# Kernel tuning notes

Measured on AMD Instinct MI355X. Metric: run time of the kernel, lower is better.

The kernel has to match this reference:

```python
import jax, jax.numpy as jnp
import numpy as np

N_NODES = 100000
N_EDGES = 1000000
HEADS = 3
NEG_SLOPE_ATTN = 0.2   # DGL EdgeGATConv default negative_slope
NEG_SLOPE_MLP = 0.01   # torch nn.LeakyReLU default


def _edge_softmax(e, dst, num_nodes):
    # softmax over incoming edges of each destination node; e: [E,H]
    m = jax.ops.segment_max(e, dst, num_segments=num_nodes)
    ex = jnp.exp(e - m[dst])
    s = jax.ops.segment_sum(ex, dst, num_segments=num_nodes)
    return ex / s[dst]


def _edge_gat(h, ef, src, dst, Wfc, Wedge, al, ar, ae, Wres, b, D):
    # Faithful to dgl.nn.EdgeGATConv (residual=True, bias=True defaults).
    N = h.shape[0]
    H = HEADS
    ft = (h @ Wfc).reshape(N, H, D)        # [N,H,D] projected node feats
    fe = (ef @ Wedge).reshape(-1, H, D)    # [E,H,D] projected edge feats
    el = jnp.einsum('nhd,hd->nh', ft, al)
    er = jnp.einsum('nhd,hd->nh', ft, ar)
    ee = jnp.einsum('ehd,hd->eh', fe, ae)
    e = jax.nn.leaky_relu(el[src] + er[dst] + ee, NEG_SLOPE_ATTN)  # [E,H]
    a = _edge_softmax(e, dst, N)                                   # [E,H]
    rst = jax.ops.segment_sum(ft[src] * a[..., None], dst, num_segments=N)
    # residual projection + bias (DGL defaults residual=True, bias=True)
    return rst + (h @ Wres).reshape(N, H, D) + b.reshape(1, H, D)


def _forward(node_feats, edge_feats,
             W1, We1, al1, ar1, ae1, Wr1, b1,
             W2, We2, al2, ar2, ae2, Wr2, b2,
             W3, We3, al3, ar3, ae3, Wr3, b3,
             L1a_w, L1a_b, L1b_w, L1b_b, L1c_w, L1c_b, L2_w, L2_b,
             src, dst):
    h1 = _edge_gat(node_feats, edge_feats, src, dst, W1, We1, al1, ar1, ae1, Wr1, b1, 8)
    h2 = _edge_gat(h1.mean(axis=1), edge_feats, src, dst, W2, We2, al2, ar2, ae2, Wr2, b2, 16)
    h3 = _edge_gat(h2.mean(axis=1), edge_feats, src, dst, W3, We3, al3, ar3, ae3, Wr3, b3, 32)
    # linear1 MLP head applied per (node, head)
    x = jax.nn.leaky_relu(h3 @ L1a_w + L1a_b, NEG_SLOPE_MLP)   # [N,H,16]
    x = jax.nn.leaky_relu(x @ L1b_w + L1b_b, NEG_SLOPE_MLP)    # [N,H,4]
    x = x @ L1c_w + L1c_b                                       # [N,H,1]
    x = x.reshape(x.shape[0], -1) @ L2_w + L2_b                 # [N,1]
    return jnp.max(x, axis=0)                                   # [1]


def setup_inputs() -> dict:
    key = jax.random.key(0)
    ks = iter(jax.random.split(key, 64))

    def nrm(shape, scale=0.1):
        return jax.random.normal(next(ks), shape, dtype=jnp.float32) * scale

    inp = {
        'node_feats': jax.random.normal(next(ks), (N_NODES, 6), dtype=jnp.float32),
        'edge_feats': jax.random.uniform(next(ks), (N_EDGES, 1), dtype=jnp.float32),
    }
    dims = [(6, 8), (8, 16), (16, 32)]
    for i, (din, dout) in enumerate(dims, start=1):
        inp[f'W{i}'] = nrm((din, HEADS * dout))
        inp[f'We{i}'] = nrm((1, HEADS * dout))
        inp[f'al{i}'] = nrm((HEADS, dout))
        inp[f'ar{i}'] = nrm((HEADS, dout))
        inp[f'ae{i}'] = nrm((HEADS, dout))
        inp[f'Wr{i}'] = nrm((din, HEADS * dout))
        inp[f'b{i}'] = nrm((HEADS * dout,))
    inp['L1a_w'] = nrm((32, 16)); inp['L1a_b'] = nrm((16,))
    inp['L1b_w'] = nrm((16, 4));  inp['L1b_b'] = nrm((4,))
    inp['L1c_w'] = nrm((4, 1));   inp['L1c_b'] = nrm((1,))
    inp['L2_w'] = nrm((HEADS, 1)); inp['L2_b'] = nrm((1,))
    inp['src'] = jax.random.randint(next(ks), (N_EDGES,), 0, N_NODES, dtype=jnp.int32)
    inp['dst'] = jax.random.randint(next(ks), (N_EDGES,), 0, N_NODES, dtype=jnp.int32)
    return inp


def reference(node_feats, edge_feats,
              W1, We1, al1, ar1, ae1, Wr1, b1,
              W2, We2, al2, ar2, ae2, Wr2, b2,
              W3, We3, al3, ar3, ae3, Wr3, b3,
              L1a_w, L1a_b, L1b_w, L1b_b, L1c_w, L1c_b, L2_w, L2_b,
              src, dst):
    return _forward(node_feats, edge_feats,
                    W1, We1, al1, ar1, ae1, Wr1, b1,
                    W2, We2, al2, ar2, ae2, Wr2, b2,
                    W3, We3, al3, ar3, ae3, Wr3, b3,
                    L1a_w, L1a_b, L1b_w, L1b_b, L1c_w, L1c_b, L2_w, L2_b,
                    src, dst)
```

## Files before the change

kernel.cpp:

```cpp
#include <hip/hip_runtime.h>
#include <hip/hip_fp16.h>
#include <math.h>

#define NN 100000
#define NE 1000000
#define NCHUNK 160
#define CHUNK (NE/NCHUNK)
#define NODE_RANGE (NN/8)
#define CAPS 32

typedef unsigned int   u32;
typedef unsigned short u16;

__device__ __forceinline__ float lrelu(float x, float sl){ return x >= 0.f ? x : sl*x; }

__device__ __forceinline__ void atomicMaxF(float* a, float v){
    if (v >= 0.f) atomicMax((int*)a, __float_as_int(v));
    else          atomicMin((unsigned int*)a, __float_as_uint(v));
}

__global__ void __launch_bounds__(256) kInit(int* __restrict__ deg, float* __restrict__ out){
    int i = blockIdx.x*256 + threadIdx.x;
    if (i < NN + 1) deg[i] = 0;
    if (i == 0) out[0] = -INFINITY;
}

__global__ void __launch_bounds__(256) kScatterX1(const int* __restrict__ src,
        const int* __restrict__ dst, const float* __restrict__ ef,
        int* __restrict__ deg, u32* __restrict__ pack,
        int* __restrict__ ovfc, int4* __restrict__ ovf){
    const int xcd  = blockIdx.x & 7;
    const int base = (blockIdx.x >> 3)*CHUNK;
    for (int e = base + threadIdx.x; e < base + CHUNK; e += 256){
        int d = __builtin_nontemporal_load(dst + e);
        if (d / NODE_RANGE == xcd){
            int s   = __builtin_nontemporal_load(src + e);
            float fv = __builtin_nontemporal_load(ef + e);
            int pos = atomicAdd(&deg[d], 1);
            if (pos < CAPS){
                u32 rec = ((u32)s << 15) | (u32)(fv*32767.f + 0.5f);
                pack[(size_t)d*CAPS + pos] = rec;
            } else {
                int o = atomicAdd(ovfc, 1);
                ovf[o] = make_int4(d, s, __float_as_int(fv), 0);
            }
        }
    }
}

template<int DIN, int DINP, int D, bool WRM>
__device__ void coefBody(const float* __restrict__ Wfc, const float* __restrict__ al,
                         const float* __restrict__ ar, const float* __restrict__ We,
                         const float* __restrict__ ae, const float* __restrict__ Wres,
                         const float* __restrict__ bias,
                         float* __restrict__ q, float* __restrict__ r, float* __restrict__ ce,
                         float* __restrict__ wrm, float* __restrict__ bm){
    int t = threadIdx.x;
    for (int i = t; i < 3*DINP; i += 256){
        int hd = i/DINP, k = i - hd*DINP;
        float qa = 0.f, ra = 0.f;
        if (k < DIN){
            for (int d = 0; d < D; ++d){
                float w = Wfc[k*3*D + hd*D + d];
                qa += w*al[hd*D+d];
                ra += w*ar[hd*D+d];
            }
        }
        q[i] = qa; r[i] = ra;
    }
    if (t < 3){
        float c = 0.f;
        for (int d = 0; d < D; ++d) c += We[t*D+d]*ae[t*D+d];
        ce[t] = c;
    }
    if (WRM){
        for (int i = t; i < DIN*D; i += 256){
            int k = i/D, d = i - k*D;
            wrm[i] = (Wres[k*3*D+d] + Wres[k*3*D+D+d] + Wres[k*3*D+2*D+d])*(1.f/3.f);
        }
        for (int i = t; i < D; i += 256)
            bm[i] = (bias[i] + bias[D+i] + bias[2*D+i])*(1.f/3.f);
    }
}

__global__ void __launch_bounds__(256) kPrep(
    const float* W1, const float* al1, const float* ar1, const float* We1,
    const float* ae1, const float* Wr1, const float* b1,
    const float* W2, const float* al2, const float* ar2, const float* We2,
    const float* ae2, const float* Wr2, const float* b2,
    const float* W3, const float* al3, const float* ar3, const float* We3,
    const float* ae3, const float* Wr3, const float* b3,
    const float* L1a_w, const float* L1a_b,
    float* coef, float* FA, float* FR, float* C0,
    const float* __restrict__ nf, u32* __restrict__ ntab1, float* __restrict__ er3a)
{
    if (blockIdx.x == 0){
        coefBody<6,8,8,true>(W1, al1, ar1, We1, ae1, Wr1, b1,
            coef+0, coef+24, coef+48, coef+52, coef+100);
    } else if (blockIdx.x == 1){
        coefBody<8,8,16,true>(W2, al2, ar2, We2, ae2, Wr2, b2,
            coef+108, coef+132, coef+156, coef+160, coef+288);
    } else if (blockIdx.x == 2){
        coefBody<16,16,32,false>(W3, al3, ar3, We3, ae3, Wr3, b3,
            coef+304, coef+352, coef+400, nullptr, nullptr);
    } else if (blockIdx.x == 3){
        int t = threadIdx.x;
        for (int i = t; i < 768; i += 256){
            int hd = i >> 8, rem = i & 255;
            int k = rem >> 4, ii = rem & 15;
            float a = 0.f, r = 0.f;
            for (int d = 0; d < 32; ++d){
                float w = L1a_w[d*16 + ii];
                a += W3[k*96 + hd*32 + d]*w;
                r += Wr3[k*96 + hd*32 + d]*w;
            }
            FA[i] = a; FR[i] = r;
        }
        if (t < 48){
            int hd = t >> 4, ii = t & 15;
            float c = L1a_b[ii];
            for (int d = 0; d < 32; ++d) c += b3[hd*32 + d]*L1a_w[d*16 + ii];
            C0[t] = c;
        }
    } else {
        __shared__ float r1s[24];
        int t = threadIdx.x;
        if (t < 24){
            int hd = t >> 3, k = t & 7;
            float ra = 0.f;
            if (k < 6)
                for (int d = 0; d < 8; ++d) ra += W1[k*24 + hd*8 + d]*ar1[hd*8 + d];
            r1s[t] = ra;
        }
        __syncthreads();
        int n = (blockIdx.x - 4)*256 + t;
        if (n >= NN) return;
        float h[6];
        #pragma unroll
        for (int k = 0; k < 6; ++k) h[k] = nf[(size_t)n*6 + k];
        __half2 p0 = __floats2half2_rn(h[0], h[1]);
        __half2 p1 = __floats2half2_rn(h[2], h[3]);
        __half2 p2 = __floats2half2_rn(h[4], h[5]);
        __half2 p3 = __floats2half2_rn(0.f, 0.f);
        uint4 row;
        row.x = *(u32*)&p0; row.y = *(u32*)&p1; row.z = *(u32*)&p2; row.w = *(u32*)&p3;
        *(uint4*)(ntab1 + (size_t)n*4) = row;
        #pragma unroll
        for (int hd = 0; hd < 3; ++hd){
            float er = 0.f;
            #pragma unroll
            for (int k = 0; k < 6; ++k) er += r1s[hd*8+k]*h[k];
            er3a[(size_t)n*3+hd] = er;
        }
    }
}

template<int DINP, int DINR, int D, bool AGG>
__global__ void __launch_bounds__(256) kNode(
    const int* __restrict__ deg, const u32* __restrict__ pack,
    const int* __restrict__ ovfc, const int4* __restrict__ ovf,
    const u32* __restrict__ ntab,
    const float* __restrict__ er3, const float* __restrict__ qc,
    const float* __restrict__ cep, const float* __restrict__ hres,
    const float* __restrict__ Wfc, const float* __restrict__ Wr2,
    const float* __restrict__ b2,
    float* __restrict__ hmean_o, u32* __restrict__ ntab_next,
    float* __restrict__ er3_next, const float* __restrict__ rnext,
    float* __restrict__ agg_o)
{
    constexpr int KS   = DINP/4;
    constexpr int ROWU = DINP/2;
    constexpr int D4   = D/4;
    const int tid  = threadIdx.x;
    const int lid  = tid & 63;
    const int lane = tid & 3;
    const int n    = (blockIdx.x*256 + tid) >> 2;
    const bool alive = n < NN;

    int dg = 0;
    float e0 = 0.f, e1 = 0.f, e2 = 0.f;
    if (alive){
        dg = deg[n]; if (dg > CAPS) dg = CAPS;
        e0 = er3[(size_t)n*3+0]; e1 = er3[(size_t)n*3+1]; e2 = er3[(size_t)n*3+2];
    }
    const float c0 = cep[0], c1 = cep[1], c2 = cep[2];
    float q[3*KS];
    #pragma unroll
    for (int hd = 0; hd < 3; ++hd)
        #pragma unroll
        for (int ks = 0; ks < KS; ++ks)
            q[hd*KS+ks] = qc[hd*DINP + lane*KS + ks];

    float acc[3*KS];
    #pragma unroll
    for (int v = 0; v < 3*KS; ++v) acc[v] = 0.f;
    float s0 = 0.f, s1 = 0.f, s2 = 0.f;

    auto rowLoad = [&](int sv, u32& w0, u32& w1){
        const u32* rp = ntab + (size_t)sv*ROWU + lane*(KS/2);
        if constexpr (KS == 2){ w0 = rp[0]; w1 = 0u; }
        else { uint2 t2 = *(const uint2*)rp; w0 = t2.x; w1 = t2.y; }
    };
    auto edgeCompute = [&](float fv, u32 w0, u32 w1){
        float hv[KS];
        float2 f = __half22float2(*(__half2*)&w0);
        hv[0] = f.x; hv[1] = f.y;
        if constexpr (KS == 4){
            f = __half22float2(*(__half2*)&w1);
            hv[2] = f.x; hv[3] = f.y;
        }
        float l0 = 0.f, l1 = 0.f, l2 = 0.f;
        #pragma unroll
        for (int ks = 0; ks < KS; ++ks){
            l0 += q[ks]*hv[ks]; l1 += q[KS+ks]*hv[ks]; l2 += q[2*KS+ks]*hv[ks];
        }
        l0 += __shfl_xor(l0,1); l0 += __shfl_xor(l0,2);
        l1 += __shfl_xor(l1,1); l1 += __shfl_xor(l1,2);
        l2 += __shfl_xor(l2,1); l2 += __shfl_xor(l2,2);
        float x0 = __expf(lrelu(l0 + e0 + c0*fv, 0.2f));
        float x1 = __expf(lrelu(l1 + e1 + c1*fv, 0.2f));
        float x2 = __expf(lrelu(l2 + e2 + c2*fv, 0.2f));
        s0 += x0; s1 += x1; s2 += x2;
        #pragma unroll
        for (int ks = 0; ks < KS; ++ks){
            acc[ks]      += x0*hv[ks];
            acc[KS+ks]   += x1*hv[ks];
            acc[2*KS+ks] += x2*hv[ks];
        }
    };

    int p = n*CAPS;
    const int re = p + dg;
    while (p + 1 < re){
        u32 ra = pack[p], rb = pack[p+1];
        u32 a0, a1, b0, b1;
        rowLoad((int)(ra >> 15), a0, a1);
        rowLoad((int)(rb >> 15), b0, b1);
        edgeCompute((float)(ra & 0x7fffu)*(1.f/32767.f), a0, a1);
        edgeCompute((float)(rb & 0x7fffu)*(1.f/32767.f), b0, b1);
        p += 2;
    }
    if (p < re){
        u32 ra = pack[p];
        u32 a0, a1;
        rowLoad((int)(ra >> 15), a0, a1);
        edgeCompute((float)(ra & 0x7fffu)*(1.f/32767.f), a0, a1);
    }

    int nov = ovfc[0];
    for (int i = 0; i < nov; ++i){
        int4 o = ovf[i];
        if (alive && o.x == n){
            u32 a0, a1;
            rowLoad(o.y, a0, a1);
            edgeCompute(__int_as_float(o.z), a0, a1);
        }
    }

    float i0 = s0 > 0.f ? 1.f/s0 : 0.f;
    float i1 = s1 > 0.f ? 1.f/s1 : 0.f;
    float i2 = s2 > 0.f ? 1.f/s2 : 0.f;
    if constexpr (!AGG){ i0 *= (1.f/3.f); i1 *= (1.f/3.f); i2 *= (1.f/3.f); }
    #pragma unroll
    for (int ks = 0; ks < KS; ++ks){
        acc[ks] *= i0; acc[KS+ks] *= i1; acc[2*KS+ks] *= i2;
    }

    if constexpr (AGG){
        if (alive){
            #pragma unroll
            for (int hd = 0; hd < 3; ++hd){
                float4 v = make_float4(acc[hd*KS+0], acc[hd*KS+1], acc[hd*KS+2], acc[hd*KS+3]);
                *(float4*)(agg_o + (size_t)n*48 + hd*16 + lane*4) = v;
            }
        }
        return;
    } else {
        float hsl[KS];
        #pragma unroll
        for (int ks = 0; ks < KS; ++ks){
            int k = lane*KS + ks;
            hsl[ks] = (alive && k < DINR) ? hres[(size_t)n*DINR + k] : 0.f;
        }
        float hm[D4];
        #pragma unroll
        for (int i = 0; i < D4; ++i) hm[i] = b2[lane*D4 + i];
        #pragma unroll
        for (int r = 0; r < 4; ++r){
            int sl = (lid & ~3) | ((lid + r) & 3);
            int kb = ((lane + r) & 3)*KS;
            float as[3*KS], hs[KS];
            #pragma unroll
            for (int v = 0; v < 3*KS; ++v) as[v] = __shfl(acc[v], sl);
            #pragma unroll
            for (int v = 0; v < KS; ++v) hs[v] = __shfl(hsl[v], sl);
            #pragma unroll
            for (int ks = 0; ks < KS; ++ks){
                int k = kb + ks;
                if (DINP == DINR || k < DINR){
                    #pragma unroll
                    for (int i = 0; i < D4; ++i){
                        int d = lane*D4 + i;
                        hm[i] += as[ks]     *Wfc[k*3*D + d]
                               + as[KS+ks]  *Wfc[k*3*D + D + d]
                               + as[2*KS+ks]*Wfc[k*3*D + 2*D + d]
                               + hs[ks]     *Wr2[k*D + d];
                    }
                }
            }
        }
        if (alive){
            #pragma unroll
            for (int i = 0; i < D4; ++i)
                hmean_o[(size_t)n*D + lane*D4 + i] = hm[i];
            #pragma unroll
            for (int w = 0; w < D4/2; ++w){
                __half2 hh = __floats2half2_rn(hm[2*w], hm[2*w+1]);
                ntab_next[(size_t)n*(D/2) + lane*(D4/2) + w] = *(u32*)&hh;
            }
        }
        float p0 = 0.f, p1 = 0.f, p2 = 0.f;
        #pragma unroll
        for (int i = 0; i < D4; ++i){
            int d = lane*D4 + i;
            p0 += rnext[0*D + d]*hm[i];
            p1 += rnext[1*D + d]*hm[i];
            p2 += rnext[2*D + d]*hm[i];
        }
        p0 += __shfl_xor(p0,1); p0 += __shfl_xor(p0,2);
        p1 += __shfl_xor(p1,1); p1 += __shfl_xor(p1,2);
        p2 += __shfl_xor(p2,1); p2 += __shfl_xor(p2,2);
        if (alive && lane < 3){
            float v = (lane == 0) ? p0 : ((lane == 1) ? p1 : p2);
            er3_next[(size_t)n*3 + lane] = v;
        }
    }
}

__global__ void __launch_bounds__(256) kFin3(
    const float* __restrict__ agg,
    const float* __restrict__ hres,
    const float* __restrict__ FAg, const float* __restrict__ FRg,
    const float* __restrict__ C0g,
    const float* __restrict__ L1b_w, const float* __restrict__ L1b_b,
    const float* __restrict__ L1c_w, const float* __restrict__ L1c_b,
    const float* __restrict__ L2_w, const float* __restrict__ L2_b,
    float* __restrict__ out)
{
    __shared__ float fa[768];
    __shared__ float fr[768];
    __shared__ float lb[64];
    __shared__ float cc[64];
    const int tid = threadIdx.x;
    for (int i = tid; i < 768; i += 256){ fa[i] = FAg[i]; fr[i] = FRg[i]; }
    if (tid < 48) cc[tid] = C0g[tid];
    if (tid < 64) lb[tid] = L1b_w[tid];
    if (tid < 4)  cc[48+tid] = L1b_b[tid];
    if (tid < 4)  cc[52+tid] = L1c_w[tid];
    if (tid == 0) cc[56] = L1c_b[0];
    if (tid < 3)  cc[57+tid] = L2_w[tid];
    if (tid == 0) cc[60] = L2_b[0];
    __syncthreads();

    const int t  = blockIdx.x*256 + tid;
    const int n  = t >> 2;
    const int hd = t & 3;
    const bool alive = n < NN;

    float y = 0.f;
    if (alive && hd < 3){
        float ag[16], hr[16];
        const float4* ag4 = (const float4*)(agg + (size_t)n*48 + hd*16);
        const float4* hr4 = (const float4*)(hres + (size_t)n*16);
        #pragma unroll
        for (int w = 0; w < 4; ++w){
            float4 a = ag4[w], h = hr4[w];
            ag[4*w]=a.x; ag[4*w+1]=a.y; ag[4*w+2]=a.z; ag[4*w+3]=a.w;
            hr[4*w]=h.x; hr[4*w+1]=h.y; hr[4*w+2]=h.z; hr[4*w+3]=h.w;
        }
        float x1[16];
        #pragma unroll
        for (int i = 0; i < 16; ++i) x1[i] = cc[hd*16 + i];
        #pragma unroll
        for (int k = 0; k < 16; ++k){
            const float a = ag[k], h = hr[k];
            const float* fap = fa + hd*256 + k*16;
            const float* frp = fr + hd*256 + k*16;
            #pragma unroll
            for (int i = 0; i < 16; ++i)
                x1[i] += a*fap[i] + h*frp[i];
        }
        #pragma unroll
        for (int i = 0; i < 16; ++i) x1[i] = lrelu(x1[i], 0.01f);
        float x2[4];
        #pragma unroll
        for (int ii = 0; ii < 4; ++ii){
            float a = cc[48+ii];
            #pragma unroll
            for (int i = 0; i < 16; ++i) a += x1[i]*lb[i*4+ii];
            x2[ii] = lrelu(a, 0.01f);
        }
        float v = cc[56];
        #pragma unroll
        for (int ii = 0; ii < 4; ++ii) v += x2[ii]*cc[52+ii];
        y = v*cc[57+hd];
    }
    y += __shfl_xor(y, 1);
    y += __shfl_xor(y, 2);
    float ymax = alive ? (y + cc[60]) : -INFINITY;

    __shared__ float red[256];
    red[tid] = ymax;
    __syncthreads();
    for (int o = 128; o > 0; o >>= 1){
        if (tid < o) red[tid] = fmaxf(red[tid], red[tid+o]);
        __syncthreads();
    }
    if (tid == 0) atomicMaxF(out, red[0]);
}

extern "C" void kernel_launch(void* const* d_in, const int* in_sizes, int n_in,
                              void* d_out, int out_size, void* d_ws, size_t ws_size,
                              hipStream_t stream) {
    const float* nf  = (const float*)d_in[0];
    const float* ef  = (const float*)d_in[1];
    const float* W1  = (const float*)d_in[2];
    const float* We1 = (const float*)d_in[3];
    const float* al1 = (const float*)d_in[4];
    const float* ar1 = (const float*)d_in[5];
    const float* ae1 = (const float*)d_in[6];
    const float* Wr1 = (const float*)d_in[7];
    const float* b1  = (const float*)d_in[8];
    const float* W2  = (const float*)d_in[9];
    const float* We2 = (const float*)d_in[10];
    const float* al2 = (const float*)d_in[11];
    const float* ar2 = (const float*)d_in[12];
    const float* ae2 = (const float*)d_in[13];
    const float* Wr2 = (const float*)d_in[14];
    const float* b2  = (const float*)d_in[15];
    const float* W3  = (const float*)d_in[16];
    const float* We3 = (const float*)d_in[17];
    const float* al3 = (const float*)d_in[18];
    const float* ar3 = (const float*)d_in[19];
    const float* ae3 = (const float*)d_in[20];
    const float* Wr3 = (const float*)d_in[21];
    const float* b3  = (const float*)d_in[22];
    const float* L1a_w = (const float*)d_in[23];
    const float* L1a_b = (const float*)d_in[24];
    const float* L1b_w = (const float*)d_in[25];
    const float* L1b_b = (const float*)d_in[26];
    const float* L1c_w = (const float*)d_in[27];
    const float* L1c_b = (const float*)d_in[28];
    const float* L2_w  = (const float*)d_in[29];
    const float* L2_b  = (const float*)d_in[30];
    const int* src = (const int*)d_in[31];
    const int* dst = (const int*)d_in[32];
    float* out = (float*)d_out;

    float* ws = (float*)d_ws;
    u32* ntab1 = (u32*)ws;
    u32* ntab2 = ntab1 + (size_t)NN*4;
    u32* ntab3 = ntab2 + (size_t)NN*4;
    float* f   = (float*)(ntab3 + (size_t)NN*8);
    float* hm2  = f;  f += (size_t)NN*8;
    float* hm3  = f;  f += (size_t)NN*16;
    float* aggb = f;  f += (size_t)NN*48;
    float* er3a = f;  f += (size_t)NN*3;
    float* er3b = f;  f += (size_t)NN*3;
    float* coef = f;  f += 512;
    float* FAb = f;  f += 768;
    float* FRb = f;  f += 768;
    float* C0b = f;  f += 64;
    int* deg  = (int*)f;
    int* ovfc = deg + NN;
    int4* ovf = (int4*)(ovfc + 4);
    u32* pack = (u32*)(ovf + 4096);

    const int gI = (NN + 1 + 255)/256;
    const int gX = NCHUNK*8;
    const int gP = 4 + (NN + 255)/256;
    const int gT = (NN*4 + 255)/256;

    kInit<<<gI,256,0,stream>>>(deg, out);

    kScatterX1<<<gX,256,0,stream>>>(src, dst, ef, deg, pack, ovfc, ovf);

    kPrep<<<gP,256,0,stream>>>(W1, al1, ar1, We1, ae1, Wr1, b1,
                               W2, al2, ar2, We2, ae2, Wr2, b2,
                               W3, al3, ar3, We3, ae3, Wr3, b3,
                               L1a_w, L1a_b, coef, FAb, FRb, C0b,
                               nf, ntab1, er3a);

    kNode<8,6,8,false><<<gT,256,0,stream>>>(deg, pack, ovfc, ovf, ntab1, er3a,
        coef+0, coef+48, nf, W1, coef+52, coef+100,
        hm2, ntab2, er3b, coef+132, nullptr);

    kNode<8,8,16,false><<<gT,256,0,stream>>>(deg, pack, ovfc, ovf, ntab2, er3b,
        coef+108, coef+156, hm2, W2, coef+160, coef+288,
        hm3, ntab3, er3a, coef+352, nullptr);

    kNode<16,16,32,true><<<gT,256,0,stream>>>(deg, pack, ovfc, ovf, ntab3, er3a,
        coef+304, coef+400, hm3, W3, nullptr, nullptr,
        nullptr, nullptr, nullptr, nullptr, aggb);

    kFin3<<<gT,256,0,stream>>>(aggb, hm3, FAb, FRb, C0b,
        L1b_w, L1b_b, L1c_w, L1c_b, L2_w, L2_b, out);
}
```

Measured before the change: 192.6 us.

## Partition edges into per-XCD buckets before scattering into CSR slots

```diff
diff --git a/kernel.cpp b/kernel.cpp
--- a/kernel.cpp
+++ b/kernel.cpp
@@ -4,13 +4,16 @@
 
 #define NN 100000
 #define NE 1000000
-#define NCHUNK 160
-#define CHUNK (NE/NCHUNK)
+#define NCHUNKP 320
+#define CHUNKP (NE/NCHUNKP)
 #define NODE_RANGE (NN/8)
 #define CAPS 32
-
-typedef unsigned int   u32;
-typedef unsigned short u16;
+#define BKCAP 160000
+#define PB 64
+
+typedef unsigned int        u32;
+typedef unsigned short      u16;
+typedef unsigned long long  u64;
 
 __device__ __forceinline__ float lrelu(float x, float sl){ return x >= 0.f ? x : sl*x; }
 
@@ -19,31 +22,64 @@
     else          atomicMin((unsigned int*)a, __float_as_uint(v));
 }
 
-__global__ void __launch_bounds__(256) kInit(int* __restrict__ deg, float* __restrict__ out){
+__global__ void __launch_bounds__(256) kInit(int* __restrict__ deg, int* __restrict__ bkcur,
+                                             float* __restrict__ out){
     int i = blockIdx.x*256 + threadIdx.x;
     if (i < NN + 1) deg[i] = 0;
+    if (i < 8) bkcur[i] = i*BKCAP;
     if (i == 0) out[0] = -INFINITY;
 }
 
-__global__ void __launch_bounds__(256) kScatterX1(const int* __restrict__ src,
+__global__ void __launch_bounds__(256) kPart(const int* __restrict__ src,
         const int* __restrict__ dst, const float* __restrict__ ef,
-        int* __restrict__ deg, u32* __restrict__ pack,
+        u64* __restrict__ bkt, int* __restrict__ bkcur){
+    __shared__ u64 stg[CHUNKP];
+    __shared__ int cnt[8], lbase[8], gofs[8], cur[8];
+    const int base = blockIdx.x*CHUNKP;
+    const int t = threadIdx.x;
+    if (t < 8) cnt[t] = 0;
+    __syncthreads();
+    for (int e = base + t; e < base + CHUNKP; e += 256)
+        atomicAdd(&cnt[dst[e]/NODE_RANGE], 1);
+    __syncthreads();
+    if (t == 0){
+        int o = 0;
+        for (int r = 0; r < 8; ++r){ lbase[r] = o; o += cnt[r]; }
+    }
+    __syncthreads();
+    if (t < 8){ cur[t] = lbase[t]; gofs[t] = atomicAdd(&bkcur[t], cnt[t]); }
+    __syncthreads();
+    for (int e = base + t; e < base + CHUNKP; e += 256){
+        int d = dst[e];
+        u32 rec = ((u32)src[e] << 15) | (u32)(ef[e]*32767.f + 0.5f);
+        int slot = atomicAdd(&cur[d/NODE_RANGE], 1);
+        stg[slot] = ((u64)(u32)d << 32) | rec;
+    }
+    __syncthreads();
+    for (int i = t; i < CHUNKP; i += 256){
+        u64 v = stg[i];
+        int r = (int)(v >> 32)/NODE_RANGE;
+        bkt[(size_t)gofs[r] + (i - lbase[r])] = v;
+    }
+}
+
+__global__ void __launch_bounds__(256) kScat2(const u64* __restrict__ bkt,
+        const int* __restrict__ bkcur, int* __restrict__ deg, u32* __restrict__ pack,
         int* __restrict__ ovfc, int4* __restrict__ ovf){
-    const int xcd  = blockIdx.x & 7;
-    const int base = (blockIdx.x >> 3)*CHUNK;
-    for (int e = base + threadIdx.x; e < base + CHUNK; e += 256){
-        int d = __builtin_nontemporal_load(dst + e);
-        if (d / NODE_RANGE == xcd){
-            int s   = __builtin_nontemporal_load(src + e);
-            float fv = __builtin_nontemporal_load(ef + e);
-            int pos = atomicAdd(&deg[d], 1);
-            if (pos < CAPS){
-                u32 rec = ((u32)s << 15) | (u32)(fv*32767.f + 0.5f);
-                pack[(size_t)d*CAPS + pos] = rec;
-            } else {
-                int o = atomicAdd(ovfc, 1);
-                ovf[o] = make_int4(d, s, __float_as_int(fv), 0);
-            }
+    const int r = blockIdx.x & 7;
+    const int j = blockIdx.x >> 3;
+    const int cnt = bkcur[r] - r*BKCAP;
+    for (int i = j*256 + threadIdx.x; i < cnt; i += PB*256){
+        u64 v = bkt[(size_t)r*BKCAP + i];
+        int d  = (int)(v >> 32);
+        u32 rec = (u32)v;
+        int pos = atomicAdd(&deg[d], 1);
+        if (pos < CAPS){
+            pack[(size_t)d*CAPS + pos] = rec;
+        } else {
+            int o = atomicAdd(ovfc, 1);
+            ovf[o] = make_int4(d, (int)(rec >> 15),
+                               __float_as_int((float)(rec & 0x7fffu)*(1.f/32767.f)), 0);
         }
     }
 }
@@ -473,23 +509,28 @@
     float* C0b = f;  f += 64;
     int* deg  = (int*)f;
     int* ovfc = deg + NN;
-    int4* ovf = (int4*)(ovfc + 4);
+    int* bkcur = ovfc + 4;
+    int4* ovf = (int4*)(bkcur + 12);
     u32* pack = (u32*)(ovf + 4096);
+    u64* bkt  = (u64*)(pack + (size_t)NN*CAPS);
+    bkt = (u64*)(((size_t)bkt + 7) & ~(size_t)7);
 
     const int gI = (NN + 1 + 255)/256;
-    const int gX = NCHUNK*8;
-    const int gP = 4 + (NN + 255)/256;
+    const int gP2 = PB*8;
+    const int gPr = 4 + (NN + 255)/256;
     const int gT = (NN*4 + 255)/256;
 
-    kInit<<<gI,256,0,stream>>>(deg, out);
-
-    kScatterX1<<<gX,256,0,stream>>>(src, dst, ef, deg, pack, ovfc, ovf);
-
-    kPrep<<<gP,256,0,stream>>>(W1, al1, ar1, We1, ae1, Wr1, b1,
-                               W2, al2, ar2, We2, ae2, Wr2, b2,
-                               W3, al3, ar3, We3, ae3, Wr3, b3,
-                               L1a_w, L1a_b, coef, FAb, FRb, C0b,
-                               nf, ntab1, er3a);
+    kInit<<<gI,256,0,stream>>>(deg, bkcur, out);
+
+    kPart<<<NCHUNKP,256,0,stream>>>(src, dst, ef, bkt, bkcur);
+
+    kScat2<<<gP2,256,0,stream>>>(bkt, bkcur, deg, pack, ovfc, ovf);
+
+    kPrep<<<gPr,256,0,stream>>>(W1, al1, ar1, We1, ae1, Wr1, b1,
+                                W2, al2, ar2, We2, ae2, Wr2, b2,
+                                W3, al3, ar3, We3, ae3, Wr3, b3,
+                                L1a_w, L1a_b, coef, FAb, FRb, C0b,
+                                nf, ntab1, er3a);
 
     kNode<8,6,8,false><<<gT,256,0,stream>>>(deg, pack, ovfc, ovf, ntab1, er3a,
         coef+0, coef+48, nf, W1, coef+52, coef+100,
```

Result: slower. 198.9 us (+3.2%).
